# Kernel tuning notes

Hardware: AMD Instinct MI355X
Metric: run time of the kernel (lower is better)

Reference implementation:

```python
import jax, jax.numpy as jnp
import numpy as np

B, S, D_IN, H = 4, 2048, 1024, 1024


def setup_inputs() -> dict:
    key = jax.random.key(0)
    k1, k2, k3 = jax.random.split(key, 3)
    qkv = jax.random.normal(k1, (B, S, D_IN), dtype=jnp.float32)
    # True = position is masked out (torch masked_fill semantics)
    attention_mask = jax.random.randint(k2, (B, S), 0, 2).astype(jnp.bool_)
    W_qkv = jax.random.normal(k3, (D_IN, 3 * H), dtype=jnp.float32) * (1.0 / np.sqrt(D_IN))
    b_qkv = jnp.zeros((3 * H,), dtype=jnp.float32)
    return {"qkv": qkv, "attention_mask": attention_mask, "W_qkv": W_qkv, "b_qkv": b_qkv}


def reference(qkv, attention_mask, W_qkv, b_qkv):
    # fused QKV projection: (B, S, 3H)
    proj = jnp.einsum("bsd,dh->bsh", qkv, W_qkv) + b_qkv
    q, k, v = jnp.split(proj, 3, axis=-1)  # each (B, S, H)
    scaling_factor = jnp.asarray(H, dtype=q.dtype) ** 0.5
    q = q * scaling_factor  # NOTE: original multiplies (not divides) by sqrt(H)
    scores = jnp.einsum("bqh,bkh->bqk", q, k)  # (B, S, S)
    # mask broadcasts over the query dim: masked keys get -inf
    neg_inf = jnp.asarray(-jnp.inf, dtype=scores.dtype)
    scores = jnp.where(attention_mask[:, None, :], neg_inf, scores)
    distributions = jax.nn.softmax(scores, axis=-1)  # dropout p=0.0 -> identity
    return jnp.einsum("bqk,bkh->bqh", distributions, v)
```

## Files before the change

kernel.cpp:

```cpp
#include <hip/hip_runtime.h>
#include <stdint.h>


#define S_LEN 2048
#define BATCH 4
#define DIN   1024
#define HDIM  1024
#define N3H   3072
#define NTOK  8192

typedef unsigned short u16;
typedef __attribute__((ext_vector_type(8))) short bf16x8;
typedef __attribute__((ext_vector_type(4))) float f32x4;
typedef __attribute__((ext_vector_type(16))) float f32x16;
typedef __attribute__((ext_vector_type(4))) unsigned short u16x4;

__device__ __forceinline__ u16 f2bf(float x) {
  union { float f; unsigned u; } c; c.f = x;
  unsigned r = c.u + 0x7fffu + ((c.u >> 16) & 1u);
  return (u16)(r >> 16);
}
__device__ __forceinline__ float bf2f(u16 h) {
  union { unsigned u; float f; } c; c.u = ((unsigned)h) << 16;
  return c.f;
}

__device__ __forceinline__ void gload16(const void* g, void* lds) {
  auto* gp = reinterpret_cast<const __attribute__((address_space(1))) void*>(
      reinterpret_cast<uintptr_t>(g));
  auto* lp = reinterpret_cast<__attribute__((address_space(3))) void*>(
      (unsigned)reinterpret_cast<uintptr_t>(lds));
  __builtin_amdgcn_global_load_lds(gp, lp, 16, 0, 0);
}

__device__ __forceinline__ void stage_tile(const u16* __restrict__ g, int ld,
                                           u16* lds, int wave, int lane) {
  const int rlane = lane >> 3;
  const int kb    = (lane & 7) ^ (rlane & 7);
#pragma unroll
  for (int h = 0; h < 4; ++h) {
    const int instr = wave * 4 + h;
    const u16* gp = g + (size_t)(instr * 8 + rlane) * ld + kb * 8;
    gload16(gp, (char*)lds + instr * 1024);
  }
}

__device__ __forceinline__ void stage_half8(const u16* __restrict__ g, int ld,
                                            u16* lds, int wave, int lane) {
  const int rlane = lane >> 3;
  const int kb    = (lane & 7) ^ (rlane & 7);
#pragma unroll
  for (int h = 0; h < 2; ++h) {
    const int instr = wave * 2 + h;
    const u16* gp = g + (size_t)(instr * 8 + rlane) * ld + kb * 8;
    gload16(gp, (char*)lds + instr * 1024);
  }
}

__device__ __forceinline__ bf16x8 frag32(const u16* t, int wq, int sub, int kh,
                                         int lane) {
  const int r5   = lane & 31;
  const int row  = wq * 64 + sub * 32 + r5;
  const int slot = (kh * 2 + (lane >> 5)) ^ (r5 & 7);
  return *(const bf16x8*)(t + row * 64 + slot * 8);
}

__device__ __forceinline__ bf16x8 dsr128(int addr) {
  bf16x8 r;
  asm volatile("ds_read_b128 %0, %1" : "=v"(r) : "v"(addr));
  return r;
}

__device__ __forceinline__ f32x16 mfma32(bf16x8 a, bf16x8 b, f32x16 c) {
  return __builtin_amdgcn_mfma_f32_32x32x16_bf16(a, b, c, 0, 0, 0);
}

__device__ __forceinline__ const u16* selA(const u16* Ah, const u16* Al, int t) {
  return (t < 32) ? Ah : Al;
}
__device__ __forceinline__ const u16* selB(const u16* Bh, const u16* Bl, int t) {
  return ((t >> 4) == 1) ? Bl : Bh;
}

template <int MODE, int BUF>
__device__ __forceinline__ void tile4(
    int t, u16* lds, f32x16 acc[4][2],
    const u16* __restrict__ Ah, const u16* __restrict__ Al,
    const u16* __restrict__ Bh, const u16* __restrict__ Bl,
    int lda, int ldb, const int (&vA)[2][4], const int (&vB)[2][4],
    int wave, int lane)
{
  bf16x8 fa[2][4], fb0[4], fb1[4];

#pragma unroll
  for (int kh = 0; kh < 4; ++kh) {
    fa[0][kh] = dsr128(vA[BUF][kh]);
    fa[1][kh] = dsr128(vA[BUF][kh] + 4096);
    fb0[kh]   = dsr128(vB[BUF][kh]);
  }
  if (MODE >= 1)
    stage_half8(selA(Ah, Al, t + 1) + (size_t)128 * lda + ((t + 1) & 15) * 64,
                lda, lds + (BUF ^ 1) * 32768 + 8192, wave, lane);
  __builtin_amdgcn_s_barrier();
  asm volatile("s_waitcnt lgkmcnt(0)" ::: "memory");
  __builtin_amdgcn_sched_barrier(0);
  __builtin_amdgcn_s_setprio(1);
#pragma unroll
  for (int kh = 0; kh < 4; ++kh) {
    acc[0][0] = mfma32(fa[0][kh], fb0[kh], acc[0][0]);
    acc[1][0] = mfma32(fa[1][kh], fb0[kh], acc[1][0]);
  }
  __builtin_amdgcn_s_setprio(0);
  __builtin_amdgcn_s_barrier();

#pragma unroll
  for (int kh = 0; kh < 4; ++kh) fb1[kh] = dsr128(vB[BUF][kh] + 4096);
  if (MODE >= 1)
    stage_half8(selB(Bh, Bl, t + 1) + (size_t)128 * ldb + ((t + 1) & 15) * 64,
                ldb, lds + (BUF ^ 1) * 32768 + 24576, wave, lane);
  __builtin_amdgcn_s_barrier();
  asm volatile("s_waitcnt lgkmcnt(0)" ::: "memory");
  __builtin_amdgcn_sched_barrier(0);
  __builtin_amdgcn_s_setprio(1);
#pragma unroll
  for (int kh = 0; kh < 4; ++kh) {
    acc[0][1] = mfma32(fa[0][kh], fb1[kh], acc[0][1]);
    acc[1][1] = mfma32(fa[1][kh], fb1[kh], acc[1][1]);
  }
  __builtin_amdgcn_s_setprio(0);
  __builtin_amdgcn_s_barrier();

#pragma unroll
  for (int kh = 0; kh < 4; ++kh) {
    fa[0][kh] = dsr128(vA[BUF][kh] + 8192);
    fa[1][kh] = dsr128(vA[BUF][kh] + 8192 + 4096);
  }
  if (MODE == 2)
    stage_half8(selB(Bh, Bl, t + 2) + ((t + 2) & 15) * 64, ldb,
                lds + BUF * 32768 + 16384, wave, lane);
  __builtin_amdgcn_s_barrier();
  asm volatile("s_waitcnt lgkmcnt(0)" ::: "memory");
  __builtin_amdgcn_sched_barrier(0);
  __builtin_amdgcn_s_setprio(1);
#pragma unroll
  for (int kh = 0; kh < 4; ++kh) {
    acc[2][0] = mfma32(fa[0][kh], fb0[kh], acc[2][0]);
    acc[3][0] = mfma32(fa[1][kh], fb0[kh], acc[3][0]);
  }
  __builtin_amdgcn_s_setprio(0);
  __builtin_amdgcn_s_barrier();

  if (MODE == 2)
    stage_half8(selA(Ah, Al, t + 2) + ((t + 2) & 15) * 64, lda,
                lds + BUF * 32768, wave, lane);
  __builtin_amdgcn_s_barrier();
  __builtin_amdgcn_s_setprio(1);
#pragma unroll
  for (int kh = 0; kh < 4; ++kh) {
    acc[2][1] = mfma32(fa[0][kh], fb1[kh], acc[2][1]);
    acc[3][1] = mfma32(fa[1][kh], fb1[kh], acc[3][1]);
  }
  __builtin_amdgcn_s_setprio(0);
  if (MODE == 2) asm volatile("s_waitcnt vmcnt(4)" ::: "memory");
  if (MODE == 1) asm volatile("s_waitcnt vmcnt(0)" ::: "memory");
  __builtin_amdgcn_s_barrier();
}

__device__ __forceinline__ void gemm256_split3(
    const u16* __restrict__ Ah, const u16* __restrict__ Al,
    const u16* __restrict__ Bh, const u16* __restrict__ Bl,
    int lda, int ldb, f32x16 acc[4][2], u16* lds,
    int wm, int wn, int wave, int lane)
{
#pragma unroll
  for (int a = 0; a < 4; ++a)
#pragma unroll
    for (int b = 0; b < 2; ++b)
#pragma unroll
      for (int r = 0; r < 16; ++r) acc[a][b][r] = 0.f;

  const int r5 = lane & 31, hi = lane >> 5, x = r5 & 7;
  const int vb = r5 * 128 + ((x ^ hi) << 4);
  const int LB = (int)(unsigned)(uintptr_t)(void*)lds;
  int vA[2][4], vB[2][4];
#pragma unroll
  for (int b = 0; b < 2; ++b)
#pragma unroll
    for (int kh = 0; kh < 4; ++kh) {
      const int vk = vb ^ (kh << 5);
      vA[b][kh] = LB + b * 65536 + wm * 16384 + vk;
      vB[b][kh] = LB + b * 65536 + 32768 + (wn >> 1) * 16384 + (wn & 1) * 8192 + vk;
    }

  stage_half8(Ah, lda, lds, wave, lane);
  stage_half8(Bh, ldb, lds + 16384, wave, lane);
  stage_half8(Ah + (size_t)128 * lda, lda, lds + 8192, wave, lane);
  stage_half8(Bh + (size_t)128 * ldb, ldb, lds + 24576, wave, lane);
  stage_half8(Bh + 64, ldb, lds + 32768 + 16384, wave, lane);
  stage_half8(Ah + 64, lda, lds + 32768, wave, lane);
  asm volatile("s_waitcnt vmcnt(4)" ::: "memory");
  __builtin_amdgcn_s_barrier();

#pragma unroll 1
  for (int t = 0; t < 46; t += 2) {
    tile4<2, 0>(t,     lds, acc, Ah, Al, Bh, Bl, lda, ldb, vA, vB, wave, lane);
    tile4<2, 1>(t + 1, lds, acc, Ah, Al, Bh, Bl, lda, ldb, vA, vB, wave, lane);
  }
  tile4<1, 0>(46, lds, acc, Ah, Al, Bh, Bl, lda, ldb, vA, vB, wave, lane);
  tile4<0, 1>(47, lds, acc, Ah, Al, Bh, Bl, lda, ldb, vA, vB, wave, lane);
}

__device__ __forceinline__ void gemm_core_plain(
    const u16* __restrict__ A, const u16* __restrict__ B,
    int lda, int ldb, int K, f32x16 acc[2][2])
{
  __shared__ __align__(16) u16 lds[2 * 8192];
  u16* aT = lds; u16* bT = lds + 8192;
  const int tid  = threadIdx.x;
  const int wave = tid >> 6, lane = tid & 63;
  const int wm = wave >> 1, wn = wave & 1;

#pragma unroll
  for (int i = 0; i < 2; ++i)
#pragma unroll
    for (int j = 0; j < 2; ++j)
#pragma unroll
      for (int r = 0; r < 16; ++r) acc[i][j][r] = 0.f;

  for (int k0 = 0; k0 < K; k0 += 64) {
    stage_tile(A + k0, lda, aT, wave, lane);
    stage_tile(B + k0, ldb, bT, wave, lane);
    __syncthreads();
#pragma unroll
    for (int kh = 0; kh < 4; ++kh) {
      bf16x8 fa[2];
#pragma unroll
      for (int i = 0; i < 2; ++i) fa[i] = frag32(aT, wm, i, kh, lane);
#pragma unroll
      for (int j = 0; j < 2; ++j) {
        const bf16x8 fb = frag32(bT, wn, j, kh, lane);
#pragma unroll
        for (int i = 0; i < 2; ++i)
          acc[i][j] = __builtin_amdgcn_mfma_f32_32x32x16_bf16(fa[i], fb, acc[i][j], 0, 0, 0);
      }
    }
    __syncthreads();
  }
}

#define ROW32(r, lane) (((r) & 3) + 8 * ((r) >> 2) + 4 * ((lane) >> 5))

__global__ void prep_mask_kernel(const unsigned char* __restrict__ m,
                                 float* __restrict__ bias) {
  __shared__ int isBool;
  if (threadIdx.x == 0) isBool = 0;
  __syncthreads();
  for (int i = threadIdx.x; i < NTOK; i += 256)
    if ((i & 3) && m[i]) isBool = 1;
  __syncthreads();
  const int stride = isBool ? 1 : 4;
  const float ninf = -__builtin_inff();
  for (int i = threadIdx.x; i < NTOK; i += 256)
    bias[i] = m[(size_t)i * stride] ? ninf : 0.f;
}

__global__ __launch_bounds__(256) void split_f32_kernel(
    const float* __restrict__ x, u16* __restrict__ hi, u16* __restrict__ lo) {
  const int i = (blockIdx.x * 256 + threadIdx.x) * 4;
  const f32x4 v = *(const f32x4*)(x + i);
  u16x4 h, l;
#pragma unroll
  for (int c = 0; c < 4; ++c) {
    h[c] = f2bf(v[c]);
    l[c] = f2bf(v[c] - bf2f(h[c]));
  }
  *(u16x4*)(hi + i) = h;
  *(u16x4*)(lo + i) = l;
}

__global__ __launch_bounds__(256) void splitWT_kernel(
    const float* __restrict__ W, u16* __restrict__ whi, u16* __restrict__ wlo) {
  __shared__ float tile[32][33];
  const int t = threadIdx.x;
  const int n0 = blockIdx.x * 32;
  const int d0 = blockIdx.y * 32;
  const int dr = t >> 3, nc = (t & 7) * 4;
  const f32x4 v = *(const f32x4*)(W + (size_t)(d0 + dr) * N3H + n0 + nc);
#pragma unroll
  for (int c = 0; c < 4; ++c) tile[dr][nc + c] = v[c];
  __syncthreads();
  const int nr = t >> 3, dc = (t & 7) * 4;
  u16x4 h, l;
#pragma unroll
  for (int c = 0; c < 4; ++c) {
    const float x = tile[dc + c][nr];
    h[c] = f2bf(x);
    l[c] = f2bf(x - bf2f(h[c]));
  }
  const size_t o = (size_t)(n0 + nr) * DIN + d0 + dc;
  *(u16x4*)(whi + o) = h;
  *(u16x4*)(wlo + o) = l;
}

__global__ __launch_bounds__(512, 2) void proj_qk256_kernel(
    const u16* __restrict__ Ahi, const u16* __restrict__ Alo,
    const u16* __restrict__ Whi, const u16* __restrict__ Wlo,
    const float* __restrict__ bias,
    u16* __restrict__ qhi, u16* __restrict__ qlo,
    u16* __restrict__ khi, u16* __restrict__ klo)
{
  __shared__ __align__(16) u16 lds[2 * 4 * 8192];
  const int bx = blockIdx.x, by = blockIdx.y;
  const int tid = threadIdx.x, wave = tid >> 6, lane = tid & 63;
  const int wm = wave >> 2, wn = wave & 3;

  f32x16 acc[4][2];
  gemm256_split3(Ahi + (size_t)by * 256 * DIN, Alo + (size_t)by * 256 * DIN,
                 Whi + (size_t)bx * 256 * DIN, Wlo + (size_t)bx * 256 * DIN,
                 DIN, DIN, acc, lds, wm, wn, wave, lane);

#pragma unroll
  for (int a = 0; a < 4; ++a) {
#pragma unroll
    for (int b = 0; b < 2; ++b) {
#pragma unroll
      for (int r = 0; r < 16; ++r) {
        const int row = by * 256 + wm * 128 + a * 32 + ROW32(r, lane);
        const int col = bx * 256 + wn * 64 + b * 32 + (lane & 31);
        const float v = acc[a][b][r] + bias[col];
        const u16 h = f2bf(v);
        const u16 l = f2bf(v - bf2f(h));
        if (col < HDIM) {
          const size_t idx = (size_t)row * HDIM + col;
          qhi[idx] = h; qlo[idx] = l;
        } else {
          const size_t idx = (size_t)row * HDIM + (col - HDIM);
          khi[idx] = h; klo[idx] = l;
        }
      }
    }
  }
}

__global__ __launch_bounds__(256, 2) void proj_v_kernel(
    const u16* __restrict__ Ahi, const u16* __restrict__ Whi,
    const float* __restrict__ bias, u16* __restrict__ vt)
{
  const int bx = blockIdx.x, by = blockIdx.y;
  f32x16 acc[2][2];
  gemm_core_plain(Ahi + (size_t)by * 128 * DIN,
                  Whi + (size_t)(2048 + bx * 128) * DIN,
                  DIN, DIN, DIN, acc);
  const int lane = threadIdx.x & 63, wave = threadIdx.x >> 6;
  const int wm = wave >> 1, wn = wave & 1;
#pragma unroll
  for (int i = 0; i < 2; ++i) {
#pragma unroll
    for (int j = 0; j < 2; ++j) {
#pragma unroll
      for (int r = 0; r < 16; ++r) {
        const int row = by * 128 + wm * 64 + i * 32 + ROW32(r, lane);
        const int b = row >> 11, s = row & 2047;
        const int hcol = bx * 128 + wn * 64 + j * 32 + (lane & 31);
        const float v = acc[i][j][r] + bias[2 * HDIM + hcol];
        vt[((size_t)b * HDIM + hcol) * S_LEN + s] = f2bf(v);
      }
    }
  }
}

__global__ __launch_bounds__(512, 2) void scores256_kernel(
    const u16* __restrict__ qhi, const u16* __restrict__ qlo,
    const u16* __restrict__ khi, const u16* __restrict__ klo,
    const float* __restrict__ maskbias, float* __restrict__ scores)
{
  __shared__ __align__(16) u16 lds[2 * 4 * 8192];
  const int id = blockIdx.x;
  const int b  = id >> 6;
  const int by = (id >> 3) & 7;
  const int bx = id & 7;
  const int tid = threadIdx.x, wave = tid >> 6, lane = tid & 63;
  const int wm = wave >> 2, wn = wave & 3;

  f32x16 acc[4][2];
  const size_t qoff = ((size_t)b * S_LEN + by * 256) * HDIM;
  const size_t koff = ((size_t)b * S_LEN + bx * 256) * HDIM;
  gemm256_split3(qhi + qoff, qlo + qoff, khi + koff, klo + koff,
                 HDIM, HDIM, acc, lds, wm, wn, wave, lane);

#pragma unroll
  for (int a = 0; a < 4; ++a) {
#pragma unroll
    for (int bj = 0; bj < 2; ++bj) {
#pragma unroll
      for (int r = 0; r < 16; ++r) {
        const int q   = by * 256 + wm * 128 + a * 32 + ROW32(r, lane);
        const int key = bx * 256 + wn * 64 + bj * 32 + (lane & 31);
        scores[((size_t)b * S_LEN + q) * S_LEN + key] =
            32.0f * acc[a][bj][r] + maskbias[b * S_LEN + key];
      }
    }
  }
}

__global__ __launch_bounds__(256) void softmax_kernel(float* __restrict__ scores) {
  const int wave = threadIdx.x >> 6, lane = threadIdx.x & 63;
  const int row = blockIdx.x * 4 + wave;
  float* srow = scores + (size_t)row * S_LEN;

  f32x4 v[8];
#pragma unroll
  for (int c = 0; c < 8; ++c) v[c] = ((const f32x4*)srow)[c * 64 + lane];

  float m = -__builtin_inff();
#pragma unroll
  for (int c = 0; c < 8; ++c)
    m = fmaxf(m, fmaxf(fmaxf(v[c][0], v[c][1]), fmaxf(v[c][2], v[c][3])));
#pragma unroll
  for (int o = 32; o > 0; o >>= 1) m = fmaxf(m, __shfl_xor(m, o));

  float s = 0.f;
#pragma unroll
  for (int c = 0; c < 8; ++c) {
#pragma unroll
    for (int e = 0; e < 4; ++e) {
      v[c][e] = __expf(v[c][e] - m);
      s += v[c][e];
    }
  }
#pragma unroll
  for (int o = 32; o > 0; o >>= 1) s += __shfl_xor(s, o);
  const float inv = 1.0f / s;

  u16* prow = (u16*)srow;
#pragma unroll
  for (int c = 0; c < 8; ++c) {
    u16x4 o4 = { f2bf(v[c][0] * inv), f2bf(v[c][1] * inv),
                 f2bf(v[c][2] * inv), f2bf(v[c][3] * inv) };
    ((u16x4*)prow)[c * 64 + lane] = o4;
  }
}

__global__ __launch_bounds__(256, 2) void pv_kernel(
    const u16* __restrict__ P, const u16* __restrict__ vt, float* __restrict__ out)
{
  const int id   = blockIdx.x;
  const int xcd  = id & 7;
  const int s    = id >> 3;
  const int b    = s >> 4;
  const int slot = s & 15;
  const int bx   = (xcd & 1) * 4 + (slot & 3);
  const int by   = (xcd >> 1) * 4 + (slot >> 2);

  f32x16 acc[2][2];
  gemm_core_plain(P + ((size_t)b * S_LEN + by * 128) * (2 * S_LEN),
                  vt + ((size_t)b * HDIM + bx * 128) * S_LEN,
                  2 * S_LEN, S_LEN, S_LEN, acc);
  const int lane = threadIdx.x & 63, wave = threadIdx.x >> 6;
  const int wm = wave >> 1, wn = wave & 1;
#pragma unroll
  for (int i = 0; i < 2; ++i) {
#pragma unroll
    for (int j = 0; j < 2; ++j) {
#pragma unroll
      for (int r = 0; r < 16; ++r) {
        const int q = by * 128 + wm * 64 + i * 32 + ROW32(r, lane);
        const int h = bx * 128 + wn * 64 + j * 32 + (lane & 31);
        out[((size_t)b * S_LEN + q) * HDIM + h] = acc[i][j][r];
      }
    }
  }
}

extern "C" void kernel_launch(void* const* d_in, const int* in_sizes, int n_in,
                              void* d_out, int out_size, void* d_ws, size_t ws_size,
                              hipStream_t stream)
{
  const float* qkv  = (const float*)d_in[0];
  const void*  mask = d_in[1];
  const float* W    = (const float*)d_in[2];
  const float* bias = (const float*)d_in[3];
  float* out = (float*)d_out;
  char* ws = (char*)d_ws;

  const size_t off_mask = 0;
  const size_t off_Whi  = 32768;
  const size_t off_Wlo  = off_Whi + (size_t)N3H * DIN * 2;
  const size_t off_Qhi  = off_Wlo + (size_t)N3H * DIN * 2;
  const size_t off_Qlo  = off_Qhi + (size_t)NTOK * HDIM * 2;
  const size_t off_Khi  = off_Qlo + (size_t)NTOK * HDIM * 2;
  const size_t off_Klo  = off_Khi + (size_t)NTOK * HDIM * 2;
  const size_t off_Vt   = off_Klo + (size_t)NTOK * HDIM * 2;
  const size_t off_A    = off_Vt + (size_t)NTOK * HDIM * 2;
  const size_t off_Alo  = off_A + (size_t)NTOK * DIN * 2;
  const size_t off_sc   = off_A;

  float* maskbias = (float*)(ws + off_mask);
  u16* Whi = (u16*)(ws + off_Whi);  u16* Wlo = (u16*)(ws + off_Wlo);
  u16* Qhi = (u16*)(ws + off_Qhi);  u16* Qlo = (u16*)(ws + off_Qlo);
  u16* Khi = (u16*)(ws + off_Khi);  u16* Klo = (u16*)(ws + off_Klo);
  u16* Vt  = (u16*)(ws + off_Vt);
  u16* Ahi = (u16*)(ws + off_A);    u16* Alo = (u16*)(ws + off_Alo);
  float* scores = (float*)(ws + off_sc);

  prep_mask_kernel<<<1, 256, 0, stream>>>((const unsigned char*)mask, maskbias);
  split_f32_kernel<<<NTOK * DIN / 1024, 256, 0, stream>>>(qkv, Ahi, Alo);
  splitWT_kernel<<<dim3(N3H / 32, DIN / 32), 256, 0, stream>>>(W, Whi, Wlo);
  proj_qk256_kernel<<<dim3(2 * HDIM / 256, NTOK / 256), 512, 0, stream>>>(
      Ahi, Alo, Whi, Wlo, bias, Qhi, Qlo, Khi, Klo);
  proj_v_kernel<<<dim3(HDIM / 128, NTOK / 128, 1), 256, 0, stream>>>(
      Ahi, Whi, bias, Vt);
  scores256_kernel<<<64 * BATCH, 512, 0, stream>>>(
      Qhi, Qlo, Khi, Klo, maskbias, scores);
  softmax_kernel<<<NTOK / 4, 256, 0, stream>>>(scores);
  pv_kernel<<<8 * 16 * BATCH, 256, 0, stream>>>(
      (const u16*)scores, Vt, out);
}
```

Measured before the change: 426.4 us.

## Restructure split-GEMM K-tile pipeline into two phases with whole-tile prefetch

Replaces the four-phase per-K-tile schedule, which staged half-tiles into LDS between barrier-separated MFMA groups, with a two-phase schedule. All B fragments and the first A fragments are read up front, and the next-next tile is staged in one block after the compute. The B LDS layout offset is simplified. This cuts the barrier count per tile from about eight to two, at the cost of higher fragment register pressure and less fine-grained overlap of global loads with MFMA work.

```diff
diff --git a/kernel.cpp b/kernel.cpp
--- a/kernel.cpp
+++ b/kernel.cpp
@@ -57,6 +57,15 @@
   }
 }
 
+__device__ __forceinline__ void stage_tile8(
+    const u16* __restrict__ A, const u16* __restrict__ B, int lda, int ldb,
+    u16* ldsbuf, int wave, int lane) {
+  stage_half8(A, lda, ldsbuf, wave, lane);
+  stage_half8(A + (size_t)128 * lda, lda, ldsbuf + 8192, wave, lane);
+  stage_half8(B, ldb, ldsbuf + 16384, wave, lane);
+  stage_half8(B + (size_t)128 * ldb, ldb, ldsbuf + 24576, wave, lane);
+}
+
 __device__ __forceinline__ bf16x8 frag32(const u16* t, int wq, int sub, int kh,
                                          int lane) {
   const int r5   = lane & 31;
@@ -83,25 +92,22 @@
 }
 
 template <int MODE, int BUF>
-__device__ __forceinline__ void tile4(
+__device__ __forceinline__ void tileK(
     int t, u16* lds, f32x16 acc[4][2],
     const u16* __restrict__ Ah, const u16* __restrict__ Al,
     const u16* __restrict__ Bh, const u16* __restrict__ Bl,
     int lda, int ldb, const int (&vA)[2][4], const int (&vB)[2][4],
     int wave, int lane)
 {
-  bf16x8 fa[2][4], fb0[4], fb1[4];
+  bf16x8 fb0[4], fb1[4], fa[2][4];
 
 #pragma unroll
   for (int kh = 0; kh < 4; ++kh) {
+    fb0[kh]   = dsr128(vB[BUF][kh]);
+    fb1[kh]   = dsr128(vB[BUF][kh] + 4096);
     fa[0][kh] = dsr128(vA[BUF][kh]);
     fa[1][kh] = dsr128(vA[BUF][kh] + 4096);
-    fb0[kh]   = dsr128(vB[BUF][kh]);
-  }
-  if (MODE >= 1)
-    stage_half8(selA(Ah, Al, t + 1) + (size_t)128 * lda + ((t + 1) & 15) * 64,
-                lda, lds + (BUF ^ 1) * 32768 + 8192, wave, lane);
-  __builtin_amdgcn_s_barrier();
+  }
   asm volatile("s_waitcnt lgkmcnt(0)" ::: "memory");
   __builtin_amdgcn_sched_barrier(0);
   __builtin_amdgcn_s_setprio(1);
@@ -109,59 +115,35 @@
   for (int kh = 0; kh < 4; ++kh) {
     acc[0][0] = mfma32(fa[0][kh], fb0[kh], acc[0][0]);
     acc[1][0] = mfma32(fa[1][kh], fb0[kh], acc[1][0]);
+    acc[0][1] = mfma32(fa[0][kh], fb1[kh], acc[0][1]);
+    acc[1][1] = mfma32(fa[1][kh], fb1[kh], acc[1][1]);
   }
   __builtin_amdgcn_s_setprio(0);
-  __builtin_amdgcn_s_barrier();
-
-#pragma unroll
-  for (int kh = 0; kh < 4; ++kh) fb1[kh] = dsr128(vB[BUF][kh] + 4096);
-  if (MODE >= 1)
-    stage_half8(selB(Bh, Bl, t + 1) + (size_t)128 * ldb + ((t + 1) & 15) * 64,
-                ldb, lds + (BUF ^ 1) * 32768 + 24576, wave, lane);
-  __builtin_amdgcn_s_barrier();
+
+#pragma unroll
+  for (int kh = 0; kh < 4; ++kh) {
+    fa[0][kh] = dsr128(vA[BUF][kh] + 8192);
+    fa[1][kh] = dsr128(vA[BUF][kh] + 12288);
+  }
   asm volatile("s_waitcnt lgkmcnt(0)" ::: "memory");
   __builtin_amdgcn_sched_barrier(0);
   __builtin_amdgcn_s_setprio(1);
 #pragma unroll
   for (int kh = 0; kh < 4; ++kh) {
-    acc[0][1] = mfma32(fa[0][kh], fb1[kh], acc[0][1]);
-    acc[1][1] = mfma32(fa[1][kh], fb1[kh], acc[1][1]);
-  }
-  __builtin_amdgcn_s_setprio(0);
-  __builtin_amdgcn_s_barrier();
-
-#pragma unroll
-  for (int kh = 0; kh < 4; ++kh) {
-    fa[0][kh] = dsr128(vA[BUF][kh] + 8192);
-    fa[1][kh] = dsr128(vA[BUF][kh] + 8192 + 4096);
-  }
-  if (MODE == 2)
-    stage_half8(selB(Bh, Bl, t + 2) + ((t + 2) & 15) * 64, ldb,
-                lds + BUF * 32768 + 16384, wave, lane);
-  __builtin_amdgcn_s_barrier();
-  asm volatile("s_waitcnt lgkmcnt(0)" ::: "memory");
-  __builtin_amdgcn_sched_barrier(0);
-  __builtin_amdgcn_s_setprio(1);
-#pragma unroll
-  for (int kh = 0; kh < 4; ++kh) {
     acc[2][0] = mfma32(fa[0][kh], fb0[kh], acc[2][0]);
     acc[3][0] = mfma32(fa[1][kh], fb0[kh], acc[3][0]);
-  }
-  __builtin_amdgcn_s_setprio(0);
-  __builtin_amdgcn_s_barrier();
-
-  if (MODE == 2)
-    stage_half8(selA(Ah, Al, t + 2) + ((t + 2) & 15) * 64, lda,
-                lds + BUF * 32768, wave, lane);
-  __builtin_amdgcn_s_barrier();
-  __builtin_amdgcn_s_setprio(1);
-#pragma unroll
-  for (int kh = 0; kh < 4; ++kh) {
     acc[2][1] = mfma32(fa[0][kh], fb1[kh], acc[2][1]);
     acc[3][1] = mfma32(fa[1][kh], fb1[kh], acc[3][1]);
   }
   __builtin_amdgcn_s_setprio(0);
-  if (MODE == 2) asm volatile("s_waitcnt vmcnt(4)" ::: "memory");
+
+  __builtin_amdgcn_s_barrier();
+  if (MODE == 2) {
+    stage_tile8(selA(Ah, Al, t + 2) + ((t + 2) & 15) * 64,
+                selB(Bh, Bl, t + 2) + ((t + 2) & 15) * 64,
+                lda, ldb, lds + BUF * 32768, wave, lane);
+    asm volatile("s_waitcnt vmcnt(8)" ::: "memory");
+  }
   if (MODE == 1) asm volatile("s_waitcnt vmcnt(0)" ::: "memory");
   __builtin_amdgcn_s_barrier();
 }
@@ -189,25 +171,21 @@
     for (int kh = 0; kh < 4; ++kh) {
       const int vk = vb ^ (kh << 5);
       vA[b][kh] = LB + b * 65536 + wm * 16384 + vk;
-      vB[b][kh] = LB + b * 65536 + 32768 + (wn >> 1) * 16384 + (wn & 1) * 8192 + vk;
-    }
-
-  stage_half8(Ah, lda, lds, wave, lane);
-  stage_half8(Bh, ldb, lds + 16384, wave, lane);
-  stage_half8(Ah + (size_t)128 * lda, lda, lds + 8192, wave, lane);
-  stage_half8(Bh + (size_t)128 * ldb, ldb, lds + 24576, wave, lane);
-  stage_half8(Bh + 64, ldb, lds + 32768 + 16384, wave, lane);
-  stage_half8(Ah + 64, lda, lds + 32768, wave, lane);
-  asm volatile("s_waitcnt vmcnt(4)" ::: "memory");
+      vB[b][kh] = LB + b * 65536 + 32768 + wn * 8192 + vk;
+    }
+
+  stage_tile8(Ah, Bh, lda, ldb, lds, wave, lane);
+  stage_tile8(Ah + 64, Bh + 64, lda, ldb, lds + 32768, wave, lane);
+  asm volatile("s_waitcnt vmcnt(8)" ::: "memory");
   __builtin_amdgcn_s_barrier();
 
 #pragma unroll 1
   for (int t = 0; t < 46; t += 2) {
-    tile4<2, 0>(t,     lds, acc, Ah, Al, Bh, Bl, lda, ldb, vA, vB, wave, lane);
-    tile4<2, 1>(t + 1, lds, acc, Ah, Al, Bh, Bl, lda, ldb, vA, vB, wave, lane);
-  }
-  tile4<1, 0>(46, lds, acc, Ah, Al, Bh, Bl, lda, ldb, vA, vB, wave, lane);
-  tile4<0, 1>(47, lds, acc, Ah, Al, Bh, Bl, lda, ldb, vA, vB, wave, lane);
+    tileK<2, 0>(t,     lds, acc, Ah, Al, Bh, Bl, lda, ldb, vA, vB, wave, lane);
+    tileK<2, 1>(t + 1, lds, acc, Ah, Al, Bh, Bl, lda, ldb, vA, vB, wave, lane);
+  }
+  tileK<1, 0>(46, lds, acc, Ah, Al, Bh, Bl, lda, ldb, vA, vB, wave, lane);
+  tileK<0, 1>(47, lds, acc, Ah, Al, Bh, Bl, lda, ldb, vA, vB, wave, lane);
 }
 
 __device__ __forceinline__ void gemm_core_plain(
```

After: 410.7 us. 3.7% less time.
